# Kernel optimization log

Hardware: AMD Instinct MI355X
Metric: run time of the kernel (lower is better)

The kernel has to match this reference:

```python
import jax, jax.numpy as jnp
import numpy as np


def setup_inputs() -> dict:
    key = jax.random.key(0)
    k1, k2, k3, k4 = jax.random.split(key, 4)
    L, B, D, H = 512, 128, 512, 1024
    x = jax.random.normal(k1, (L, B, D), dtype=jnp.float32)
    Wx = jax.random.normal(k2, (H, D), dtype=jnp.float32) * (1.0 / np.sqrt(D))
    bx = jax.random.normal(k3, (H,), dtype=jnp.float32) * 0.01
    Wh = jax.random.normal(k4, (H, H), dtype=jnp.float32) * (1.0 / np.sqrt(H))
    return {"x": x, "Wx": Wx, "bx": bx, "Wh": Wh}


def reference(x, Wx, bx, Wh):
    # x: [L, B, D]; Wx: [H, D]; bx: [H]; Wh: [H, H]
    # h_t = tanh(x_t @ Wx^T + bx + h_{t-1} @ Wh^T), h_{-1} = 0
    L, B, D = x.shape
    H = Wx.shape[0]
    # Precompute the input projection for all timesteps in one big GEMM.
    xproj = jnp.einsum('lbd,hd->lbh', x, Wx) + bx  # [L, B, H]

    def step(h, xp_t):
        h_new = jnp.tanh(xp_t + h @ Wh.T)  # [B, H]
        return h_new, h_new

    h0 = jnp.zeros((B, H), dtype=x.dtype)
    _, hs = jax.lax.scan(step, h0, xproj)
    return hs  # [L, B, H]
```

## Files before the change

kernel.cpp:

```cpp
#include <hip/hip_runtime.h>
#include <math.h>


#define L_SEQ 512
#define B_SZ  128
#define D_SZ  512
#define H_SZ  1024
#define BH    (B_SZ * H_SZ)

typedef __bf16 bf16x8 __attribute__((ext_vector_type(8)));
typedef float  f32x4  __attribute__((ext_vector_type(4)));
typedef unsigned int uint;

union V8 { bf16x8 b; unsigned short u[8]; uint w[4]; };

__device__ __forceinline__ unsigned short f2bf(float f) {
  unsigned int u = __float_as_uint(f);
  u += 0x7FFFu + ((u >> 16) & 1u);
  return (unsigned short)(u >> 16);
}
__device__ __forceinline__ float bf2f(unsigned short s) {
  return __uint_as_float(((unsigned int)s) << 16);
}

__device__ __forceinline__ float fast_tanh(float x) {
  float e;
  asm("v_exp_f32 %0, %1" : "=v"(e) : "v"(x * 2.885390081777927f));
  float r;
  asm("v_rcp_f32 %0, %1" : "=v"(r) : "v"(e + 1.0f));
  return 1.0f - 2.0f * r;
}

__device__ __forceinline__ void ldg16_sc(bf16x8& d, const unsigned short* p) {
  asm volatile("global_load_dwordx4 %0, %1, off sc0 sc1"
               : "=v"(d) : "v"(p) : "memory");
}
__device__ __forceinline__ void stg2_sc(unsigned short* p, uint v) {
  asm volatile("global_store_short %0, %1, off sc0 sc1"
               :: "v"(p), "v"(v) : "memory");
}
__device__ __forceinline__ void stg4_sc(uint* p, uint v) {
  asm volatile("global_store_dword %0, %1, off sc0 sc1"
               :: "v"(p), "v"(v) : "memory");
}

#define WS_WHH 0
#define WS_WHL 1048576
#define WS_WXH 2097152
#define WS_WXL 2621440
#define WS_HB  3145728
#define WS_CNT 3670016

__global__ void split_kernel(const float* __restrict__ Wh,
                             const float* __restrict__ Wx,
                             unsigned short* __restrict__ ws,
                             unsigned int* __restrict__ flags) {
  if (blockIdx.x == 0) {
    for (int i = threadIdx.x; i < 512; i += 256) flags[i] = 0u;
  }
  const int total = 1048576 + 524288;
  for (int i = blockIdx.x * blockDim.x + threadIdx.x; i < total;
       i += gridDim.x * blockDim.x) {
    const float* src; unsigned short *dh, *dl; int j;
    if (i < 1048576) { src = Wh; dh = ws + WS_WHH; dl = ws + WS_WHL; j = i; }
    else             { src = Wx; dh = ws + WS_WXH; dl = ws + WS_WXL; j = i - 1048576; }
    float v = src[j];
    unsigned short h = f2bf(v);
    dh[j] = h;
    dl[j] = f2bf(v - bf2f(h));
  }
}

__global__ __launch_bounds__(256) void xproj_kernel(
    const float* __restrict__ x,
    const unsigned short* __restrict__ wxh,
    const unsigned short* __restrict__ wxl,
    const float* __restrict__ bx,
    float* __restrict__ out)
{
  const int bid = blockIdx.x;
  const int bn = bid & 15;
  const int bm = bid >> 4;
  const int tid = threadIdx.x;
  const int w = tid >> 6, l = tid & 63;
  const int wm = w & 1, wn = w >> 1;
  const int lr = l & 15, lk = (l >> 4) * 8;
  const int mbase = bm * 128 + wm * 64;
  const int nbase = bn * 64 + wn * 32;

  f32x4 acc[4][2] = {};

  for (int k0 = 0; k0 < 512; k0 += 32) {
    bf16x8 ah[4], al[4], bh[2], bl[2];
#pragma unroll
    for (int i = 0; i < 4; ++i) {
      const float* ap = x + (size_t)(mbase + i * 16 + lr) * 512 + k0 + lk;
      float4 v0 = *reinterpret_cast<const float4*>(ap);
      float4 v1 = *reinterpret_cast<const float4*>(ap + 4);
      float vv[8] = {v0.x, v0.y, v0.z, v0.w, v1.x, v1.y, v1.z, v1.w};
      V8 hh, ll;
#pragma unroll
      for (int e = 0; e < 8; ++e) {
        unsigned short hb = f2bf(vv[e]);
        hh.u[e] = hb;
        ll.u[e] = f2bf(vv[e] - bf2f(hb));
      }
      ah[i] = hh.b; al[i] = ll.b;
    }
#pragma unroll
    for (int j = 0; j < 2; ++j) {
      size_t boff = (size_t)(nbase + j * 16 + lr) * 512 + k0 + lk;
      bh[j] = *reinterpret_cast<const bf16x8*>(wxh + boff);
      bl[j] = *reinterpret_cast<const bf16x8*>(wxl + boff);
    }
#pragma unroll
    for (int i = 0; i < 4; ++i)
#pragma unroll
      for (int j = 0; j < 2; ++j) {
        acc[i][j] = __builtin_amdgcn_mfma_f32_16x16x32_bf16(ah[i], bh[j], acc[i][j], 0, 0, 0);
        acc[i][j] = __builtin_amdgcn_mfma_f32_16x16x32_bf16(ah[i], bl[j], acc[i][j], 0, 0, 0);
        acc[i][j] = __builtin_amdgcn_mfma_f32_16x16x32_bf16(al[i], bh[j], acc[i][j], 0, 0, 0);
      }
  }

#pragma unroll
  for (int j = 0; j < 2; ++j) {
    int n = nbase + j * 16 + lr;
    float bxv = bx[n];
#pragma unroll
    for (int i = 0; i < 4; ++i)
#pragma unroll
      for (int r = 0; r < 4; ++r) {
        int m = mbase + i * 16 + (l >> 4) * 4 + r;
        out[(size_t)m * 1024 + n] = acc[i][j][r] + bxv;
      }
  }
}

__global__ __launch_bounds__(512, 2) void rnn_persistent(
    const unsigned short* __restrict__ whh,
    const unsigned short* __restrict__ whl,
    unsigned short* __restrict__ hb,
    float* __restrict__ out,
    uint* __restrict__ flags)
{
  __shared__ float lds[8 * 32 * 17];
  const int wg = blockIdx.x;
  const int xc = wg & 7, yy = wg >> 3;
  const int mb = xc & 3;
  const int nb = ((xc >> 2) << 5) + yy;
  const int tid = threadIdx.x;
  const int q = tid >> 6;
  const int l = tid & 63;
  const int lr = l & 15, lk = (l >> 4) * 8;
  const int kbase = q * 128 + lk;
  const int row0 = (l >> 4) * 4;

  const unsigned short* bph = whh + (size_t)(nb * 16 + lr) * 1024 + kbase;
  const unsigned short* bpl = whl + (size_t)(nb * 16 + lr) * 1024 + kbase;
  bf16x8 vBh[4], vBl[4];
#pragma unroll
  for (int kb = 0; kb < 4; ++kb) {
    vBh[kb] = *reinterpret_cast<const bf16x8*>(bph + kb * 32);
    vBl[kb] = *reinterpret_cast<const bf16x8*>(bpl + kb * 32);
  }

  const size_t aoff = (size_t)(mb * 32 + lr) * 1024 + kbase;
  const unsigned short* planeA0 = hb + aoff;
  const unsigned short* planeA1 = hb + 2 * BH + aoff;

  const int em = tid >> 4, en = tid & 15;
  const size_t eidx = (size_t)(mb * 32 + em) * 1024 + nb * 16 + en;

  const uint* gate_ptr = flags + (mb << 6) + (q << 3) + (l & 7);
  uint* my_flag = flags + (mb << 6) + nb;

  for (int t = 0; t < L_SEQ; ++t) {
    float* xpt = out + (size_t)t * BH;
    const float xpv = xpt[eidx];
    float hval;

    if (t > 0) {
      const uint tgt = (uint)t;
      for (uint spin = 0; spin < (1u << 22); ++spin) {
        uint f;
        asm volatile("global_load_dword %0, %1, off sc0 sc1\n\t"
                     "s_waitcnt vmcnt(0)"
                     : "=v"(f) : "v"(gate_ptr) : "memory");
        if (__all((int)(f >= tgt))) break;
        __builtin_amdgcn_s_sleep(1);
      }
      __builtin_amdgcn_sched_barrier(0);

      const unsigned short* ah = ((t - 1) & 1) ? planeA1 : planeA0;
      const unsigned short* al = ah + BH;
      bf16x8 vA0h[4], vA0l[4], vA1h[4], vA1l[4];
#pragma unroll
      for (int kb = 0; kb < 4; ++kb) {
        const int ko = kb * 32;
        ldg16_sc(vA0h[kb], ah + ko);
        ldg16_sc(vA0l[kb], al + ko);
        ldg16_sc(vA1h[kb], ah + 16 * 1024 + ko);
        ldg16_sc(vA1l[kb], al + 16 * 1024 + ko);
      }
      asm volatile("s_waitcnt vmcnt(0)" ::: "memory");
      __builtin_amdgcn_sched_barrier(0);

      f32x4 acc0 = {0.f, 0.f, 0.f, 0.f};
      f32x4 acc1 = {0.f, 0.f, 0.f, 0.f};
#pragma unroll
      for (int kb = 0; kb < 4; ++kb) {
        acc0 = __builtin_amdgcn_mfma_f32_16x16x32_bf16(vA0h[kb], vBh[kb], acc0, 0, 0, 0);
        acc1 = __builtin_amdgcn_mfma_f32_16x16x32_bf16(vA1h[kb], vBh[kb], acc1, 0, 0, 0);
        acc0 = __builtin_amdgcn_mfma_f32_16x16x32_bf16(vA0h[kb], vBl[kb], acc0, 0, 0, 0);
        acc1 = __builtin_amdgcn_mfma_f32_16x16x32_bf16(vA1h[kb], vBl[kb], acc1, 0, 0, 0);
        acc0 = __builtin_amdgcn_mfma_f32_16x16x32_bf16(vA0l[kb], vBh[kb], acc0, 0, 0, 0);
        acc1 = __builtin_amdgcn_mfma_f32_16x16x32_bf16(vA1l[kb], vBh[kb], acc1, 0, 0, 0);
      }

#pragma unroll
      for (int r = 0; r < 4; ++r) {
        lds[q * 544 + (row0 + r) * 17 + lr]      = acc0[r];
        lds[q * 544 + (16 + row0 + r) * 17 + lr] = acc1[r];
      }
      __syncthreads();

      float s = 0.f;
#pragma unroll
      for (int qq = 0; qq < 8; ++qq) s += lds[qq * 544 + em * 17 + en];
      hval = fast_tanh(s + xpv);
    } else {
      hval = fast_tanh(xpv);
    }

    unsigned short hhi = f2bf(hval);
    unsigned short hlo = f2bf(hval - bf2f(hhi));
    unsigned short* hcur = hb + (size_t)((t & 1) * 2) * BH;
    stg2_sc(hcur + eidx, (uint)hhi);
    stg2_sc(hcur + BH + eidx, (uint)hlo);
    asm volatile("s_waitcnt vmcnt(0)" ::: "memory");
    __syncthreads();
    if (tid == 0) stg4_sc(my_flag, (uint)(t + 1));

    xpt[eidx] = hval;
  }
}

extern "C" void kernel_launch(void* const* d_in, const int* in_sizes, int n_in,
                              void* d_out, int out_size, void* d_ws, size_t ws_size,
                              hipStream_t stream) {
  const float* x  = (const float*)d_in[0];
  const float* Wx = (const float*)d_in[1];
  const float* bx = (const float*)d_in[2];
  const float* Wh = (const float*)d_in[3];
  float* out = (float*)d_out;
  unsigned short* ws = (unsigned short*)d_ws;

  unsigned short* whh = ws + WS_WHH;
  unsigned short* whl = ws + WS_WHL;
  unsigned short* wxh = ws + WS_WXH;
  unsigned short* wxl = ws + WS_WXL;
  unsigned short* hb  = ws + WS_HB;
  uint* flags         = (uint*)(ws + WS_CNT);

  split_kernel<<<dim3(2048), dim3(256), 0, stream>>>(Wh, Wx, ws, flags);
  xproj_kernel<<<dim3(8192), dim3(256), 0, stream>>>(x, wxh, wxl, bx, out);
  rnn_persistent<<<dim3(256), dim3(512), 0, stream>>>(whh, whl, hb, out, flags);
}
```

Measured before the change: 3.700 ms.

## Interleave two batch chains per workgroup to overlap flag waits with compute

The persistent RNN kernel now launches 128 workgroups instead of 256. Each one owns a column block for two batch slices and alternates between them within each timestep. Gating is split per slice, and flags are published early, so one slice's matmul can proceed while the other slice's dependencies are still arriving. The goal is to hide cross-workgroup synchronization latency, at the cost of halving parallelism, serializing two chains per workgroup, and adding a more delicate flag-ordering protocol. The spin limit is also reduced.

```diff
diff --git a/kernel.cpp b/kernel.cpp
--- a/kernel.cpp
+++ b/kernel.cpp
@@ -4,7 +4,6 @@
 
 #define L_SEQ 512
 #define B_SZ  128
-#define D_SZ  512
 #define H_SZ  1024
 #define BH    (B_SZ * H_SZ)
 
@@ -12,7 +11,7 @@
 typedef float  f32x4  __attribute__((ext_vector_type(4)));
 typedef unsigned int uint;
 
-union V8 { bf16x8 b; unsigned short u[8]; uint w[4]; };
+union V8 { bf16x8 b; unsigned short u[8]; };
 
 __device__ __forceinline__ unsigned short f2bf(float f) {
   unsigned int u = __float_as_uint(f);
@@ -34,6 +33,12 @@
 __device__ __forceinline__ void ldg16_sc(bf16x8& d, const unsigned short* p) {
   asm volatile("global_load_dwordx4 %0, %1, off sc0 sc1"
                : "=v"(d) : "v"(p) : "memory");
+}
+__device__ __forceinline__ uint ld4w_sc(const uint* p) {
+  uint f;
+  asm volatile("global_load_dword %0, %1, off sc0 sc1\n\ts_waitcnt vmcnt(0)"
+               : "=v"(f) : "v"(p) : "memory");
+  return f;
 }
 __device__ __forceinline__ void stg2_sc(unsigned short* p, uint v) {
   asm volatile("global_store_short %0, %1, off sc0 sc1"
@@ -146,9 +151,9 @@
 {
   __shared__ float lds[8 * 32 * 17];
   const int wg = blockIdx.x;
-  const int xc = wg & 7, yy = wg >> 3;
-  const int mb = xc & 3;
-  const int nb = ((xc >> 2) << 5) + yy;
+  const int p  = wg & 1;
+  const int nb = wg >> 1;
+  const int mbA = 2 * p, mbB = 2 * p + 1;
   const int tid = threadIdx.x;
   const int q = tid >> 6;
   const int l = tid & 63;
@@ -165,84 +170,102 @@
     vBl[kb] = *reinterpret_cast<const bf16x8*>(bpl + kb * 32);
   }
 
-  const size_t aoff = (size_t)(mb * 32 + lr) * 1024 + kbase;
-  const unsigned short* planeA0 = hb + aoff;
-  const unsigned short* planeA1 = hb + 2 * BH + aoff;
-
+  const size_t aoffA = (size_t)(mbA * 32 + lr) * 1024 + kbase;
+  const size_t aoffB = (size_t)(mbB * 32 + lr) * 1024 + kbase;
   const int em = tid >> 4, en = tid & 15;
-  const size_t eidx = (size_t)(mb * 32 + em) * 1024 + nb * 16 + en;
-
-  const uint* gate_ptr = flags + (mb << 6) + (q << 3) + (l & 7);
-  uint* my_flag = flags + (mb << 6) + nb;
-
-  for (int t = 0; t < L_SEQ; ++t) {
-    float* xpt = out + (size_t)t * BH;
-    const float xpv = xpt[eidx];
-    float hval;
-
-    if (t > 0) {
-      const uint tgt = (uint)t;
-      for (uint spin = 0; spin < (1u << 22); ++spin) {
-        uint f;
-        asm volatile("global_load_dword %0, %1, off sc0 sc1\n\t"
-                     "s_waitcnt vmcnt(0)"
-                     : "=v"(f) : "v"(gate_ptr) : "memory");
-        if (__all((int)(f >= tgt))) break;
-        __builtin_amdgcn_s_sleep(1);
-      }
-      __builtin_amdgcn_sched_barrier(0);
-
-      const unsigned short* ah = ((t - 1) & 1) ? planeA1 : planeA0;
-      const unsigned short* al = ah + BH;
-      bf16x8 vA0h[4], vA0l[4], vA1h[4], vA1l[4];
-#pragma unroll
-      for (int kb = 0; kb < 4; ++kb) {
-        const int ko = kb * 32;
-        ldg16_sc(vA0h[kb], ah + ko);
-        ldg16_sc(vA0l[kb], al + ko);
-        ldg16_sc(vA1h[kb], ah + 16 * 1024 + ko);
-        ldg16_sc(vA1l[kb], al + 16 * 1024 + ko);
-      }
-      asm volatile("s_waitcnt vmcnt(0)" ::: "memory");
-      __builtin_amdgcn_sched_barrier(0);
-
-      f32x4 acc0 = {0.f, 0.f, 0.f, 0.f};
-      f32x4 acc1 = {0.f, 0.f, 0.f, 0.f};
-#pragma unroll
-      for (int kb = 0; kb < 4; ++kb) {
-        acc0 = __builtin_amdgcn_mfma_f32_16x16x32_bf16(vA0h[kb], vBh[kb], acc0, 0, 0, 0);
-        acc1 = __builtin_amdgcn_mfma_f32_16x16x32_bf16(vA1h[kb], vBh[kb], acc1, 0, 0, 0);
-        acc0 = __builtin_amdgcn_mfma_f32_16x16x32_bf16(vA0h[kb], vBl[kb], acc0, 0, 0, 0);
-        acc1 = __builtin_amdgcn_mfma_f32_16x16x32_bf16(vA1h[kb], vBl[kb], acc1, 0, 0, 0);
-        acc0 = __builtin_amdgcn_mfma_f32_16x16x32_bf16(vA0l[kb], vBh[kb], acc0, 0, 0, 0);
-        acc1 = __builtin_amdgcn_mfma_f32_16x16x32_bf16(vA1l[kb], vBh[kb], acc1, 0, 0, 0);
-      }
-
-#pragma unroll
-      for (int r = 0; r < 4; ++r) {
-        lds[q * 544 + (row0 + r) * 17 + lr]      = acc0[r];
-        lds[q * 544 + (16 + row0 + r) * 17 + lr] = acc1[r];
-      }
-      __syncthreads();
-
-      float s = 0.f;
-#pragma unroll
-      for (int qq = 0; qq < 8; ++qq) s += lds[qq * 544 + em * 17 + en];
-      hval = fast_tanh(s + xpv);
-    } else {
-      hval = fast_tanh(xpv);
-    }
-
-    unsigned short hhi = f2bf(hval);
-    unsigned short hlo = f2bf(hval - bf2f(hhi));
+  const size_t eidxA = (size_t)(mbA * 32 + em) * 1024 + nb * 16 + en;
+  const size_t eidxB = (size_t)(mbB * 32 + em) * 1024 + nb * 16 + en;
+  const uint* gateA = flags + (mbA << 6) + (q << 3) + (l & 7);
+  const uint* gateB = flags + (mbB << 6) + (q << 3) + (l & 7);
+  uint* myA = flags + (mbA << 6) + nb;
+  uint* myB = flags + (mbB << 6) + nb;
+
+  auto chain_mm = [&](const size_t aoff, int t, float xpv) -> float {
+    const unsigned short* ah = hb + (size_t)(((t - 1) & 1) * 2) * BH + aoff;
+    const unsigned short* al = ah + BH;
+    bf16x8 vA0h[4], vA0l[4], vA1h[4], vA1l[4];
+#pragma unroll
+    for (int kb = 0; kb < 4; ++kb) {
+      const int ko = kb * 32;
+      ldg16_sc(vA0h[kb], ah + ko);
+      ldg16_sc(vA0l[kb], al + ko);
+      ldg16_sc(vA1h[kb], ah + 16 * 1024 + ko);
+      ldg16_sc(vA1l[kb], al + 16 * 1024 + ko);
+    }
+    asm volatile("s_waitcnt vmcnt(0)" ::: "memory");
+    __builtin_amdgcn_sched_barrier(0);
+
+    f32x4 a0 = {0.f, 0.f, 0.f, 0.f};
+    f32x4 a1 = {0.f, 0.f, 0.f, 0.f};
+#pragma unroll
+    for (int kb = 0; kb < 4; ++kb) {
+      a0 = __builtin_amdgcn_mfma_f32_16x16x32_bf16(vA0h[kb], vBh[kb], a0, 0, 0, 0);
+      a1 = __builtin_amdgcn_mfma_f32_16x16x32_bf16(vA1h[kb], vBh[kb], a1, 0, 0, 0);
+      a0 = __builtin_amdgcn_mfma_f32_16x16x32_bf16(vA0h[kb], vBl[kb], a0, 0, 0, 0);
+      a1 = __builtin_amdgcn_mfma_f32_16x16x32_bf16(vA1h[kb], vBl[kb], a1, 0, 0, 0);
+      a0 = __builtin_amdgcn_mfma_f32_16x16x32_bf16(vA0l[kb], vBh[kb], a0, 0, 0, 0);
+      a1 = __builtin_amdgcn_mfma_f32_16x16x32_bf16(vA1l[kb], vBh[kb], a1, 0, 0, 0);
+    }
+#pragma unroll
+    for (int r = 0; r < 4; ++r) {
+      lds[q * 544 + (row0 + r) * 17 + lr]      = a0[r];
+      lds[q * 544 + (16 + row0 + r) * 17 + lr] = a1[r];
+    }
+    __syncthreads();
+    float s = 0.f;
+#pragma unroll
+    for (int qq = 0; qq < 8; ++qq) s += lds[qq * 544 + em * 17 + en];
+    return fast_tanh(s + xpv);
+  };
+
+  auto store_h = [&](int t, size_t eidx, float h) {
+    unsigned short hhi = f2bf(h);
+    unsigned short hlo = f2bf(h - bf2f(hhi));
     unsigned short* hcur = hb + (size_t)((t & 1) * 2) * BH;
     stg2_sc(hcur + eidx, (uint)hhi);
     stg2_sc(hcur + BH + eidx, (uint)hlo);
+  };
+
+  auto gate = [&](const uint* gp, uint tgt) {
+    for (uint spin = 0; spin < (1u << 20); ++spin) {
+      uint f = ld4w_sc(gp);
+      if (__all((int)(f >= tgt))) break;
+      __builtin_amdgcn_s_sleep(1);
+    }
+    __builtin_amdgcn_sched_barrier(0);
+  };
+
+  {
+    float hA = fast_tanh(out[eidxA]);
+    float hB = fast_tanh(out[eidxB]);
+    store_h(0, eidxA, hA);
+    store_h(0, eidxB, hB);
+    out[eidxA] = hA;
+    out[eidxB] = hB;
     asm volatile("s_waitcnt vmcnt(0)" ::: "memory");
     __syncthreads();
-    if (tid == 0) stg4_sc(my_flag, (uint)(t + 1));
-
-    xpt[eidx] = hval;
+    if (tid == 0) { stg4_sc(myA, 1u); stg4_sc(myB, 1u); }
+  }
+
+  for (int t = 1; t < L_SEQ; ++t) {
+    float* xpt = out + (size_t)t * BH;
+    const float xpvA = xpt[eidxA];
+    const float xpvB = xpt[eidxB];
+
+    gate(gateA, (uint)t);
+    __syncthreads();
+    if (tid == 0) stg4_sc(myB, (uint)t);
+    float hA = chain_mm(aoffA, t, xpvA);
+    store_h(t, eidxA, hA);
+
+    gate(gateB, (uint)t);
+    __syncthreads();
+    if (tid == 0) stg4_sc(myA, (uint)(t + 1));
+    float hB = chain_mm(aoffB, t, xpvB);
+    store_h(t, eidxB, hB);
+
+    xpt[eidxA] = hA;
+    xpt[eidxB] = hB;
   }
 }
 
@@ -265,5 +288,5 @@
 
   split_kernel<<<dim3(2048), dim3(256), 0, stream>>>(Wh, Wx, ws, flags);
   xproj_kernel<<<dim3(8192), dim3(256), 0, stream>>>(x, wxh, wxl, bx, out);
-  rnn_persistent<<<dim3(256), dim3(512), 0, stream>>>(whh, whl, hb, out, flags);
-}
+  rnn_persistent<<<dim3(128), dim3(512), 0, stream>>>(whh, whl, hb, out, flags);
+}
```

New measurement: 5.773 ms. 56.0% more time.

## Replace flag barriers with timestep-tagged hidden-state words polled directly

Applied to the files above, without the earlier changes.

Each hidden-state element is now stored as an 8-byte word: the packed bf16 hi/lo pair plus the timestep tag. Consumers poll the data itself until every tag matches, which removes the separate flag store and flag poll round trip from each step. Work is redistributed across 128 workgroups, each owning 16 batch rows by 64 hidden columns over the full K. Fetched rows are transposed into LDS, MFMAs run per wave, and partial sums are reduced through LDS. The tag buffer reuses the Wx split region. This adds per-step polling traffic, and correctness depends on stale tags never matching the current timestep.

```diff
diff --git a/kernel.cpp b/kernel.cpp
--- a/kernel.cpp
+++ b/kernel.cpp
@@ -4,23 +4,25 @@
 
 #define L_SEQ 512
 #define B_SZ  128
-#define D_SZ  512
 #define H_SZ  1024
 #define BH    (B_SZ * H_SZ)
 
 typedef __bf16 bf16x8 __attribute__((ext_vector_type(8)));
 typedef float  f32x4  __attribute__((ext_vector_type(4)));
 typedef unsigned int uint;
-
-union V8 { bf16x8 b; unsigned short u[8]; uint w[4]; };
-
-__device__ __forceinline__ unsigned short f2bf(float f) {
-  unsigned int u = __float_as_uint(f);
+typedef uint u32x4 __attribute__((ext_vector_type(4)));
+typedef uint u32x2 __attribute__((ext_vector_type(2)));
+typedef unsigned short ushort;
+
+union V8 { bf16x8 b; ushort u[8]; };
+
+__device__ __forceinline__ ushort f2bf(float f) {
+  uint u = __float_as_uint(f);
   u += 0x7FFFu + ((u >> 16) & 1u);
-  return (unsigned short)(u >> 16);
-}
-__device__ __forceinline__ float bf2f(unsigned short s) {
-  return __uint_as_float(((unsigned int)s) << 16);
+  return (ushort)(u >> 16);
+}
+__device__ __forceinline__ float bf2f(ushort s) {
+  return __uint_as_float(((uint)s) << 16);
 }
 
 __device__ __forceinline__ float fast_tanh(float x) {
@@ -31,16 +33,12 @@
   return 1.0f - 2.0f * r;
 }
 
-__device__ __forceinline__ void ldg16_sc(bf16x8& d, const unsigned short* p) {
+__device__ __forceinline__ void ldg16_sc(u32x4& d, const uint* p) {
   asm volatile("global_load_dwordx4 %0, %1, off sc0 sc1"
                : "=v"(d) : "v"(p) : "memory");
 }
-__device__ __forceinline__ void stg2_sc(unsigned short* p, uint v) {
-  asm volatile("global_store_short %0, %1, off sc0 sc1"
-               :: "v"(p), "v"(v) : "memory");
-}
-__device__ __forceinline__ void stg4_sc(uint* p, uint v) {
-  asm volatile("global_store_dword %0, %1, off sc0 sc1"
+__device__ __forceinline__ void stg8_sc(uint* p, u32x2 v) {
+  asm volatile("global_store_dwordx2 %0, %1, off sc0 sc1"
                :: "v"(p), "v"(v) : "memory");
 }
 
@@ -48,24 +46,18 @@
 #define WS_WHL 1048576
 #define WS_WXH 2097152
 #define WS_WXL 2621440
-#define WS_HB  3145728
-#define WS_CNT 3670016
 
 __global__ void split_kernel(const float* __restrict__ Wh,
                              const float* __restrict__ Wx,
-                             unsigned short* __restrict__ ws,
-                             unsigned int* __restrict__ flags) {
-  if (blockIdx.x == 0) {
-    for (int i = threadIdx.x; i < 512; i += 256) flags[i] = 0u;
-  }
+                             ushort* __restrict__ ws) {
   const int total = 1048576 + 524288;
   for (int i = blockIdx.x * blockDim.x + threadIdx.x; i < total;
        i += gridDim.x * blockDim.x) {
-    const float* src; unsigned short *dh, *dl; int j;
+    const float* src; ushort *dh, *dl; int j;
     if (i < 1048576) { src = Wh; dh = ws + WS_WHH; dl = ws + WS_WHL; j = i; }
     else             { src = Wx; dh = ws + WS_WXH; dl = ws + WS_WXL; j = i - 1048576; }
     float v = src[j];
-    unsigned short h = f2bf(v);
+    ushort h = f2bf(v);
     dh[j] = h;
     dl[j] = f2bf(v - bf2f(h));
   }
@@ -73,8 +65,8 @@
 
 __global__ __launch_bounds__(256) void xproj_kernel(
     const float* __restrict__ x,
-    const unsigned short* __restrict__ wxh,
-    const unsigned short* __restrict__ wxl,
+    const ushort* __restrict__ wxh,
+    const ushort* __restrict__ wxl,
     const float* __restrict__ bx,
     float* __restrict__ out)
 {
@@ -101,7 +93,7 @@
       V8 hh, ll;
 #pragma unroll
       for (int e = 0; e < 8; ++e) {
-        unsigned short hb = f2bf(vv[e]);
+        ushort hb = f2bf(vv[e]);
         hh.u[e] = hb;
         ll.u[e] = f2bf(vv[e] - bf2f(hb));
       }
@@ -138,111 +130,133 @@
 }
 
 __global__ __launch_bounds__(512, 2) void rnn_persistent(
-    const unsigned short* __restrict__ whh,
-    const unsigned short* __restrict__ whl,
-    unsigned short* __restrict__ hb,
-    float* __restrict__ out,
-    uint* __restrict__ flags)
+    const ushort* __restrict__ whh,
+    const ushort* __restrict__ whl,
+    uint* __restrict__ hbt,
+    float* __restrict__ out)
 {
-  __shared__ float lds[8 * 32 * 17];
+  __shared__ uint smraw[16384];
+  ushort* lds_hi = (ushort*)smraw;
+  ushort* lds_lo = lds_hi + 16384;
+  float*  part   = (float*)smraw;
+
   const int wg = blockIdx.x;
-  const int xc = wg & 7, yy = wg >> 3;
-  const int mb = xc & 3;
-  const int nb = ((xc >> 2) << 5) + yy;
+  const int g  = wg & 7;
+  const int c  = wg >> 3;
   const int tid = threadIdx.x;
-  const int q = tid >> 6;
-  const int l = tid & 63;
-  const int lr = l & 15, lk = (l >> 4) * 8;
-  const int kbase = q * 128 + lk;
-  const int row0 = (l >> 4) * 4;
-
-  const unsigned short* bph = whh + (size_t)(nb * 16 + lr) * 1024 + kbase;
-  const unsigned short* bpl = whl + (size_t)(nb * 16 + lr) * 1024 + kbase;
-  bf16x8 vBh[4], vBl[4];
-#pragma unroll
-  for (int kb = 0; kb < 4; ++kb) {
-    vBh[kb] = *reinterpret_cast<const bf16x8*>(bph + kb * 32);
-    vBl[kb] = *reinterpret_cast<const bf16x8*>(bpl + kb * 32);
-  }
-
-  const size_t aoff = (size_t)(mb * 32 + lr) * 1024 + kbase;
-  const unsigned short* planeA0 = hb + aoff;
-  const unsigned short* planeA1 = hb + 2 * BH + aoff;
-
-  const int em = tid >> 4, en = tid & 15;
-  const size_t eidx = (size_t)(mb * 32 + em) * 1024 + nb * 16 + en;
-
-  const uint* gate_ptr = flags + (mb << 6) + (q << 3) + (l & 7);
-  uint* my_flag = flags + (mb << 6) + nb;
-
-  for (int t = 0; t < L_SEQ; ++t) {
+  const int w = tid >> 6, l = tid & 63;
+  const int lr = l & 15, lq = l >> 4;
+
+  bf16x8 vBh[4][4], vBl[4][4];
+#pragma unroll
+  for (int ct = 0; ct < 4; ++ct)
+#pragma unroll
+    for (int ck = 0; ck < 4; ++ck) {
+      size_t a = (size_t)(c * 64 + ct * 16 + lr) * 1024 + w * 128 + ck * 32 + lq * 8;
+      vBh[ct][ck] = *reinterpret_cast<const bf16x8*>(whh + a);
+      vBl[ct][ck] = *reinterpret_cast<const bf16x8*>(whl + a);
+    }
+
+  const int e0 = tid * 2;
+  const int row0 = e0 >> 6, cw0 = e0 & 63;
+  const int row1 = (e0 + 1) >> 6, cw1 = (e0 + 1) & 63;
+  const size_t oidx0 = (size_t)(g * 16 + row0) * 1024 + c * 64 + cw0;
+  const size_t oidx1 = (size_t)(g * 16 + row1) * 1024 + c * 64 + cw1;
+
+  const uint* pollbase[2];
+  pollbase[0] = hbt + (((size_t)g * 16384 + w * 2048 + l * 2) << 1);
+  pollbase[1] = hbt + (((size_t)BH + g * 16384 + w * 2048 + l * 2) << 1);
+
+  {
+    float h0 = fast_tanh(out[oidx0]);
+    float h1 = fast_tanh(out[oidx1]);
+    out[oidx0] = h0;
+    out[oidx1] = h1;
+    ushort hh0 = f2bf(h0), hh1 = f2bf(h1);
+    u32x2 v0, v1;
+    v0[0] = ((uint)hh0 << 16) | (uint)f2bf(h0 - bf2f(hh0)); v0[1] = 1u;
+    v1[0] = ((uint)hh1 << 16) | (uint)f2bf(h1 - bf2f(hh1)); v1[1] = 1u;
+    stg8_sc(hbt + (oidx0 << 1), v0);
+    stg8_sc(hbt + (oidx1 << 1), v1);
+  }
+
+  for (int t = 1; t < L_SEQ; ++t) {
     float* xpt = out + (size_t)t * BH;
-    const float xpv = xpt[eidx];
-    float hval;
-
-    if (t > 0) {
-      const uint tgt = (uint)t;
-      for (uint spin = 0; spin < (1u << 22); ++spin) {
-        uint f;
-        asm volatile("global_load_dword %0, %1, off sc0 sc1\n\t"
-                     "s_waitcnt vmcnt(0)"
-                     : "=v"(f) : "v"(gate_ptr) : "memory");
-        if (__all((int)(f >= tgt))) break;
-        __builtin_amdgcn_s_sleep(1);
-      }
-      __builtin_amdgcn_sched_barrier(0);
-
-      const unsigned short* ah = ((t - 1) & 1) ? planeA1 : planeA0;
-      const unsigned short* al = ah + BH;
-      bf16x8 vA0h[4], vA0l[4], vA1h[4], vA1l[4];
-#pragma unroll
-      for (int kb = 0; kb < 4; ++kb) {
-        const int ko = kb * 32;
-        ldg16_sc(vA0h[kb], ah + ko);
-        ldg16_sc(vA0l[kb], al + ko);
-        ldg16_sc(vA1h[kb], ah + 16 * 1024 + ko);
-        ldg16_sc(vA1l[kb], al + 16 * 1024 + ko);
-      }
+    const float xpv0 = xpt[oidx0];
+    const float xpv1 = xpt[oidx1];
+
+    const uint* pb = pollbase[(t - 1) & 1];
+    const uint tg = (uint)t;
+    u32x4 d[16];
+    for (uint spin = 0; spin < (1u << 20); ++spin) {
+      #pragma unroll
+      for (int i = 0; i < 16; ++i) ldg16_sc(d[i], pb + (i << 8));
       asm volatile("s_waitcnt vmcnt(0)" ::: "memory");
       __builtin_amdgcn_sched_barrier(0);
-
-      f32x4 acc0 = {0.f, 0.f, 0.f, 0.f};
-      f32x4 acc1 = {0.f, 0.f, 0.f, 0.f};
-#pragma unroll
-      for (int kb = 0; kb < 4; ++kb) {
-        acc0 = __builtin_amdgcn_mfma_f32_16x16x32_bf16(vA0h[kb], vBh[kb], acc0, 0, 0, 0);
-        acc1 = __builtin_amdgcn_mfma_f32_16x16x32_bf16(vA1h[kb], vBh[kb], acc1, 0, 0, 0);
-        acc0 = __builtin_amdgcn_mfma_f32_16x16x32_bf16(vA0h[kb], vBl[kb], acc0, 0, 0, 0);
-        acc1 = __builtin_amdgcn_mfma_f32_16x16x32_bf16(vA1h[kb], vBl[kb], acc1, 0, 0, 0);
-        acc0 = __builtin_amdgcn_mfma_f32_16x16x32_bf16(vA0l[kb], vBh[kb], acc0, 0, 0, 0);
-        acc1 = __builtin_amdgcn_mfma_f32_16x16x32_bf16(vA1l[kb], vBh[kb], acc1, 0, 0, 0);
-      }
-
-#pragma unroll
-      for (int r = 0; r < 4; ++r) {
-        lds[q * 544 + (row0 + r) * 17 + lr]      = acc0[r];
-        lds[q * 544 + (16 + row0 + r) * 17 + lr] = acc1[r];
-      }
-      __syncthreads();
-
-      float s = 0.f;
-#pragma unroll
-      for (int qq = 0; qq < 8; ++qq) s += lds[qq * 544 + em * 17 + en];
-      hval = fast_tanh(s + xpv);
-    } else {
-      hval = fast_tanh(xpv);
-    }
-
-    unsigned short hhi = f2bf(hval);
-    unsigned short hlo = f2bf(hval - bf2f(hhi));
-    unsigned short* hcur = hb + (size_t)((t & 1) * 2) * BH;
-    stg2_sc(hcur + eidx, (uint)hhi);
-    stg2_sc(hcur + BH + eidx, (uint)hlo);
-    asm volatile("s_waitcnt vmcnt(0)" ::: "memory");
+      bool ok = true;
+      #pragma unroll
+      for (int i = 0; i < 16; ++i) ok = ok && (d[i][1] == tg) && (d[i][3] == tg);
+      if (__all((int)ok)) break;
+      __builtin_amdgcn_s_sleep(1);
+    }
+    __builtin_amdgcn_sched_barrier(0);
+
+    #pragma unroll
+    for (int i = 0; i < 16; ++i) {
+      const int e = w * 2048 + i * 128 + l * 2;
+      const int row = e >> 10, k = e & 1023;
+      const int u = ((k >> 3) << 4) + row;
+      const int pos = k & 7;
+      uint hip = (d[i][0] >> 16) | (d[i][2] & 0xFFFF0000u);
+      uint lop = (d[i][0] & 0xFFFFu) | (d[i][2] << 16);
+      *reinterpret_cast<uint*>(lds_hi + u * 8 + pos) = hip;
+      *reinterpret_cast<uint*>(lds_lo + u * 8 + pos) = lop;
+    }
     __syncthreads();
-    if (tid == 0) stg4_sc(my_flag, (uint)(t + 1));
-
-    xpt[eidx] = hval;
+
+    bf16x8 vAh[4], vAl[4];
+    #pragma unroll
+    for (int ck = 0; ck < 4; ++ck) {
+      const int u = ((w * 16 + ck * 4 + lq) << 4) + lr;
+      vAh[ck] = *reinterpret_cast<const bf16x8*>(lds_hi + u * 8);
+      vAl[ck] = *reinterpret_cast<const bf16x8*>(lds_lo + u * 8);
+    }
+    __syncthreads();
+
+    f32x4 acc[4] = {};
+    #pragma unroll
+    for (int ct = 0; ct < 4; ++ct)
+      #pragma unroll
+      for (int ck = 0; ck < 4; ++ck) {
+        acc[ct] = __builtin_amdgcn_mfma_f32_16x16x32_bf16(vAh[ck], vBh[ct][ck], acc[ct], 0, 0, 0);
+        acc[ct] = __builtin_amdgcn_mfma_f32_16x16x32_bf16(vAh[ck], vBl[ct][ck], acc[ct], 0, 0, 0);
+        acc[ct] = __builtin_amdgcn_mfma_f32_16x16x32_bf16(vAl[ck], vBh[ct][ck], acc[ct], 0, 0, 0);
+      }
+
+    #pragma unroll
+    for (int ct = 0; ct < 4; ++ct)
+      #pragma unroll
+      for (int r = 0; r < 4; ++r)
+        part[w * 1088 + (ct * 16 + lr) * 17 + lq * 4 + r] = acc[ct][r];
+    __syncthreads();
+
+    float s0 = 0.f, s1 = 0.f;
+    #pragma unroll
+    for (int q = 0; q < 8; ++q) {
+      s0 += part[q * 1088 + cw0 * 17 + row0];
+      s1 += part[q * 1088 + cw1 * 17 + row1];
+    }
+    float h0 = fast_tanh(s0 + xpv0);
+    float h1 = fast_tanh(s1 + xpv1);
+    ushort hh0 = f2bf(h0), hh1 = f2bf(h1);
+    u32x2 v0, v1;
+    v0[0] = ((uint)hh0 << 16) | (uint)f2bf(h0 - bf2f(hh0)); v0[1] = tg + 1u;
+    v1[0] = ((uint)hh1 << 16) | (uint)f2bf(h1 - bf2f(hh1)); v1[1] = tg + 1u;
+    uint* planew = hbt + ((size_t)(t & 1) * BH << 1);
+    stg8_sc(planew + (oidx0 << 1), v0);
+    stg8_sc(planew + (oidx1 << 1), v1);
+    xpt[oidx0] = h0;
+    xpt[oidx1] = h1;
   }
 }
 
@@ -254,16 +268,15 @@
   const float* bx = (const float*)d_in[2];
   const float* Wh = (const float*)d_in[3];
   float* out = (float*)d_out;
-  unsigned short* ws = (unsigned short*)d_ws;
-
-  unsigned short* whh = ws + WS_WHH;
-  unsigned short* whl = ws + WS_WHL;
-  unsigned short* wxh = ws + WS_WXH;
-  unsigned short* wxl = ws + WS_WXL;
-  unsigned short* hb  = ws + WS_HB;
-  uint* flags         = (uint*)(ws + WS_CNT);
-
-  split_kernel<<<dim3(2048), dim3(256), 0, stream>>>(Wh, Wx, ws, flags);
+  ushort* ws = (ushort*)d_ws;
+
+  ushort* whh = ws + WS_WHH;
+  ushort* whl = ws + WS_WHL;
+  ushort* wxh = ws + WS_WXH;
+  ushort* wxl = ws + WS_WXL;
+  uint*   hbt = (uint*)(ws + WS_WXH);
+
+  split_kernel<<<dim3(2048), dim3(256), 0, stream>>>(Wh, Wx, ws);
   xproj_kernel<<<dim3(8192), dim3(256), 0, stream>>>(x, wxh, wxl, bx, out);
-  rnn_persistent<<<dim3(256), dim3(512), 0, stream>>>(whh, whl, hb, out, flags);
-}
+  rnn_persistent<<<dim3(128), dim3(512), 0, stream>>>(whh, whl, hbt, out);
+}
```

Result: slower. 4.150 ms (+12.2%).

## Fuse input projection GEMM into persistent RNN kernel with per-timestep readiness flags

Applied to the files above, without the earlier changes.

Merges the input-projection GEMM and the persistent recurrence into one launch. The first 256 blocks run the recurrence; the remaining blocks compute projection tiles in timestep order and publish a flag per tile. Recurrence blocks spin on both the neighbour step flags and the matching projection flag before reading that step's projection. The aim is to overlap the projection with the early timesteps and drop a kernel boundary. The projection blocks share CUs with the latency-bound recurrence and may slow its steps, and the design relies on the persistent blocks all being resident while the producer blocks still make progress.

```diff
diff --git a/kernel.cpp b/kernel.cpp
--- a/kernel.cpp
+++ b/kernel.cpp
@@ -4,23 +4,23 @@
 
 #define L_SEQ 512
 #define B_SZ  128
-#define D_SZ  512
 #define H_SZ  1024
 #define BH    (B_SZ * H_SZ)
 
 typedef __bf16 bf16x8 __attribute__((ext_vector_type(8)));
 typedef float  f32x4  __attribute__((ext_vector_type(4)));
 typedef unsigned int uint;
-
-union V8 { bf16x8 b; unsigned short u[8]; uint w[4]; };
-
-__device__ __forceinline__ unsigned short f2bf(float f) {
-  unsigned int u = __float_as_uint(f);
+typedef unsigned short ushort;
+
+union V8 { bf16x8 b; ushort u[8]; uint w[4]; };
+
+__device__ __forceinline__ ushort f2bf(float f) {
+  uint u = __float_as_uint(f);
   u += 0x7FFFu + ((u >> 16) & 1u);
-  return (unsigned short)(u >> 16);
-}
-__device__ __forceinline__ float bf2f(unsigned short s) {
-  return __uint_as_float(((unsigned int)s) << 16);
+  return (ushort)(u >> 16);
+}
+__device__ __forceinline__ float bf2f(ushort s) {
+  return __uint_as_float(((uint)s) << 16);
 }
 
 __device__ __forceinline__ float fast_tanh(float x) {
@@ -31,11 +31,11 @@
   return 1.0f - 2.0f * r;
 }
 
-__device__ __forceinline__ void ldg16_sc(bf16x8& d, const unsigned short* p) {
+__device__ __forceinline__ void ldg16_sc(bf16x8& d, const ushort* p) {
   asm volatile("global_load_dwordx4 %0, %1, off sc0 sc1"
                : "=v"(d) : "v"(p) : "memory");
 }
-__device__ __forceinline__ void stg2_sc(unsigned short* p, uint v) {
+__device__ __forceinline__ void stg2_sc(ushort* p, uint v) {
   asm volatile("global_store_short %0, %1, off sc0 sc1"
                :: "v"(p), "v"(v) : "memory");
 }
@@ -49,115 +49,108 @@
 #define WS_WXH 2097152
 #define WS_WXL 2621440
 #define WS_HB  3145728
-#define WS_CNT 3670016
+#define WS_FLG 3670016
 
 __global__ void split_kernel(const float* __restrict__ Wh,
                              const float* __restrict__ Wx,
-                             unsigned short* __restrict__ ws,
-                             unsigned int* __restrict__ flags) {
-  if (blockIdx.x == 0) {
-    for (int i = threadIdx.x; i < 512; i += 256) flags[i] = 0u;
-  }
+                             ushort* __restrict__ ws,
+                             uint* __restrict__ flg) {
+  const int gid = blockIdx.x * blockDim.x + threadIdx.x;
+  if (gid < 256 + 8192) flg[gid] = 0u;
   const int total = 1048576 + 524288;
-  for (int i = blockIdx.x * blockDim.x + threadIdx.x; i < total;
-       i += gridDim.x * blockDim.x) {
-    const float* src; unsigned short *dh, *dl; int j;
+  for (int i = gid; i < total; i += gridDim.x * blockDim.x) {
+    const float* src; ushort *dh, *dl; int j;
     if (i < 1048576) { src = Wh; dh = ws + WS_WHH; dl = ws + WS_WHL; j = i; }
     else             { src = Wx; dh = ws + WS_WXH; dl = ws + WS_WXL; j = i - 1048576; }
     float v = src[j];
-    unsigned short h = f2bf(v);
+    ushort h = f2bf(v);
     dh[j] = h;
     dl[j] = f2bf(v - bf2f(h));
   }
 }
 
-__global__ __launch_bounds__(256) void xproj_kernel(
+__global__ __launch_bounds__(512, 4) void fused_kernel(
     const float* __restrict__ x,
-    const unsigned short* __restrict__ wxh,
-    const unsigned short* __restrict__ wxl,
+    const ushort* __restrict__ wxh,
+    const ushort* __restrict__ wxl,
     const float* __restrict__ bx,
-    float* __restrict__ out)
+    const ushort* __restrict__ whh,
+    const ushort* __restrict__ whl,
+    ushort* __restrict__ hb,
+    float* __restrict__ out,
+    uint* __restrict__ flags,
+    uint* __restrict__ xpflags)
 {
+  __shared__ float lds[8 * 32 * 17];
   const int bid = blockIdx.x;
-  const int bn = bid & 15;
-  const int bm = bid >> 4;
   const int tid = threadIdx.x;
-  const int w = tid >> 6, l = tid & 63;
-  const int wm = w & 1, wn = w >> 1;
-  const int lr = l & 15, lk = (l >> 4) * 8;
-  const int mbase = bm * 128 + wm * 64;
-  const int nbase = bn * 64 + wn * 32;
-
-  f32x4 acc[4][2] = {};
-
-  for (int k0 = 0; k0 < 512; k0 += 32) {
-    bf16x8 ah[4], al[4], bh[2], bl[2];
-#pragma unroll
-    for (int i = 0; i < 4; ++i) {
-      const float* ap = x + (size_t)(mbase + i * 16 + lr) * 512 + k0 + lk;
-      float4 v0 = *reinterpret_cast<const float4*>(ap);
-      float4 v1 = *reinterpret_cast<const float4*>(ap + 4);
-      float vv[8] = {v0.x, v0.y, v0.z, v0.w, v1.x, v1.y, v1.z, v1.w};
-      V8 hh, ll;
-#pragma unroll
-      for (int e = 0; e < 8; ++e) {
-        unsigned short hb = f2bf(vv[e]);
-        hh.u[e] = hb;
-        ll.u[e] = f2bf(vv[e] - bf2f(hb));
-      }
-      ah[i] = hh.b; al[i] = ll.b;
+
+  if (bid >= 256) {
+    const int xb = bid - 256;
+    const int bn = xb & 15;
+    const int bm = xb >> 4;
+    const int w = tid >> 6, l = tid & 63;
+    const int wm = w & 1, wn = w >> 1;
+    const int lr = l & 15, lk = (l >> 4) * 8;
+    const int mbase = bm * 128 + wm * 64;
+    const int nbase = bn * 64 + wn * 16;
+
+    f32x4 acc[4] = {};
+    for (int k0 = 0; k0 < 512; k0 += 32) {
+      bf16x8 ah[4], al[4], bh, bl;
+#pragma unroll
+      for (int i = 0; i < 4; ++i) {
+        const float* ap = x + (size_t)(mbase + i * 16 + lr) * 512 + k0 + lk;
+        float4 v0 = *reinterpret_cast<const float4*>(ap);
+        float4 v1 = *reinterpret_cast<const float4*>(ap + 4);
+        float vv[8] = {v0.x, v0.y, v0.z, v0.w, v1.x, v1.y, v1.z, v1.w};
+        V8 hh, ll;
+#pragma unroll
+        for (int e = 0; e < 8; ++e) {
+          ushort hbv = f2bf(vv[e]);
+          hh.u[e] = hbv;
+          ll.u[e] = f2bf(vv[e] - bf2f(hbv));
+        }
+        ah[i] = hh.b; al[i] = ll.b;
+      }
+      size_t boff = (size_t)(nbase + lr) * 512 + k0 + lk;
+      bh = *reinterpret_cast<const bf16x8*>(wxh + boff);
+      bl = *reinterpret_cast<const bf16x8*>(wxl + boff);
+#pragma unroll
+      for (int i = 0; i < 4; ++i) {
+        acc[i] = __builtin_amdgcn_mfma_f32_16x16x32_bf16(ah[i], bh, acc[i], 0, 0, 0);
+        acc[i] = __builtin_amdgcn_mfma_f32_16x16x32_bf16(ah[i], bl, acc[i], 0, 0, 0);
+        acc[i] = __builtin_amdgcn_mfma_f32_16x16x32_bf16(al[i], bh, acc[i], 0, 0, 0);
+      }
     }
-#pragma unroll
-    for (int j = 0; j < 2; ++j) {
-      size_t boff = (size_t)(nbase + j * 16 + lr) * 512 + k0 + lk;
-      bh[j] = *reinterpret_cast<const bf16x8*>(wxh + boff);
-      bl[j] = *reinterpret_cast<const bf16x8*>(wxl + boff);
-    }
-#pragma unroll
-    for (int i = 0; i < 4; ++i)
-#pragma unroll
-      for (int j = 0; j < 2; ++j) {
-        acc[i][j] = __builtin_amdgcn_mfma_f32_16x16x32_bf16(ah[i], bh[j], acc[i][j], 0, 0, 0);
-        acc[i][j] = __builtin_amdgcn_mfma_f32_16x16x32_bf16(ah[i], bl[j], acc[i][j], 0, 0, 0);
-        acc[i][j] = __builtin_amdgcn_mfma_f32_16x16x32_bf16(al[i], bh[j], acc[i][j], 0, 0, 0);
-      }
-  }
-
-#pragma unroll
-  for (int j = 0; j < 2; ++j) {
-    int n = nbase + j * 16 + lr;
-    float bxv = bx[n];
+    const int n = nbase + lr;
+    const float bxv = bx[n];
 #pragma unroll
     for (int i = 0; i < 4; ++i)
 #pragma unroll
       for (int r = 0; r < 4; ++r) {
         int m = mbase + i * 16 + (l >> 4) * 4 + r;
-        out[(size_t)m * 1024 + n] = acc[i][j][r] + bxv;
-      }
-  }
-}
-
-__global__ __launch_bounds__(512, 2) void rnn_persistent(
-    const unsigned short* __restrict__ whh,
-    const unsigned short* __restrict__ whl,
-    unsigned short* __restrict__ hb,
-    float* __restrict__ out,
-    uint* __restrict__ flags)
-{
-  __shared__ float lds[8 * 32 * 17];
-  const int wg = blockIdx.x;
+        stg4_sc((uint*)(out + (size_t)m * 1024 + n),
+                __float_as_uint(acc[i][r] + bxv));
+      }
+    asm volatile("s_waitcnt vmcnt(0)" ::: "memory");
+    __syncthreads();
+    if (tid == 0) stg4_sc(xpflags + bm * 16 + bn, 1u);
+    return;
+  }
+
+  const int wg = bid;
   const int xc = wg & 7, yy = wg >> 3;
   const int mb = xc & 3;
   const int nb = ((xc >> 2) << 5) + yy;
-  const int tid = threadIdx.x;
   const int q = tid >> 6;
   const int l = tid & 63;
   const int lr = l & 15, lk = (l >> 4) * 8;
   const int kbase = q * 128 + lk;
   const int row0 = (l >> 4) * 4;
 
-  const unsigned short* bph = whh + (size_t)(nb * 16 + lr) * 1024 + kbase;
-  const unsigned short* bpl = whl + (size_t)(nb * 16 + lr) * 1024 + kbase;
+  const ushort* bph = whh + (size_t)(nb * 16 + lr) * 1024 + kbase;
+  const ushort* bpl = whl + (size_t)(nb * 16 + lr) * 1024 + kbase;
   bf16x8 vBh[4], vBl[4];
 #pragma unroll
   for (int kb = 0; kb < 4; ++kb) {
@@ -166,8 +159,8 @@
   }
 
   const size_t aoff = (size_t)(mb * 32 + lr) * 1024 + kbase;
-  const unsigned short* planeA0 = hb + aoff;
-  const unsigned short* planeA1 = hb + 2 * BH + aoff;
+  const ushort* planeA0 = hb + aoff;
+  const ushort* planeA1 = hb + 2 * BH + aoff;
 
   const int em = tid >> 4, en = tid & 15;
   const size_t eidx = (size_t)(mb * 32 + em) * 1024 + nb * 16 + en;
@@ -176,24 +169,44 @@
   uint* my_flag = flags + (mb << 6) + nb;
 
   for (int t = 0; t < L_SEQ; ++t) {
-    float* xpt = out + (size_t)t * BH;
-    const float xpv = xpt[eidx];
+    const uint* xpf_ptr = xpflags + t * 16 + (nb >> 2);
     float hval;
 
-    if (t > 0) {
-      const uint tgt = (uint)t;
-      for (uint spin = 0; spin < (1u << 22); ++spin) {
-        uint f;
+    if (t == 0) {
+      for (uint spin = 0; spin < (1u << 20); ++spin) {
+        uint xf;
         asm volatile("global_load_dword %0, %1, off sc0 sc1\n\t"
                      "s_waitcnt vmcnt(0)"
-                     : "=v"(f) : "v"(gate_ptr) : "memory");
-        if (__all((int)(f >= tgt))) break;
+                     : "=v"(xf) : "v"(xpf_ptr) : "memory");
+        if (__all((int)(xf != 0u))) break;
         __builtin_amdgcn_s_sleep(1);
       }
       __builtin_amdgcn_sched_barrier(0);
-
-      const unsigned short* ah = ((t - 1) & 1) ? planeA1 : planeA0;
-      const unsigned short* al = ah + BH;
+      uint xu;
+      asm volatile("global_load_dword %0, %1, off sc0 sc1\n\t"
+                   "s_waitcnt vmcnt(0)"
+                   : "=v"(xu) : "v"((const uint*)(out + eidx)) : "memory");
+      hval = fast_tanh(__uint_as_float(xu));
+    } else {
+      const uint tgt = (uint)t;
+      for (uint spin = 0; spin < (1u << 20); ++spin) {
+        uint f, xf;
+        asm volatile("global_load_dword %0, %2, off sc0 sc1\n\t"
+                     "global_load_dword %1, %3, off sc0 sc1\n\t"
+                     "s_waitcnt vmcnt(0)"
+                     : "=&v"(f), "=&v"(xf)
+                     : "v"(gate_ptr), "v"(xpf_ptr) : "memory");
+        if (__all((int)((f >= tgt) & (xf != 0u)))) break;
+        __builtin_amdgcn_s_sleep(1);
+      }
+      __builtin_amdgcn_sched_barrier(0);
+
+      uint xu;
+      asm volatile("global_load_dword %0, %1, off sc0 sc1"
+                   : "=v"(xu)
+                   : "v"((const uint*)(out + (size_t)t * BH + eidx)) : "memory");
+      const ushort* ah = ((t - 1) & 1) ? planeA1 : planeA0;
+      const ushort* al = ah + BH;
       bf16x8 vA0h[4], vA0l[4], vA1h[4], vA1l[4];
 #pragma unroll
       for (int kb = 0; kb < 4; ++kb) {
@@ -228,21 +241,19 @@
       float s = 0.f;
 #pragma unroll
       for (int qq = 0; qq < 8; ++qq) s += lds[qq * 544 + em * 17 + en];
-      hval = fast_tanh(s + xpv);
-    } else {
-      hval = fast_tanh(xpv);
+      hval = fast_tanh(s + __uint_as_float(xu));
     }
 
-    unsigned short hhi = f2bf(hval);
-    unsigned short hlo = f2bf(hval - bf2f(hhi));
-    unsigned short* hcur = hb + (size_t)((t & 1) * 2) * BH;
+    ushort hhi = f2bf(hval);
+    ushort hlo = f2bf(hval - bf2f(hhi));
+    ushort* hcur = hb + (size_t)((t & 1) * 2) * BH;
     stg2_sc(hcur + eidx, (uint)hhi);
     stg2_sc(hcur + BH + eidx, (uint)hlo);
     asm volatile("s_waitcnt vmcnt(0)" ::: "memory");
     __syncthreads();
     if (tid == 0) stg4_sc(my_flag, (uint)(t + 1));
 
-    xpt[eidx] = hval;
+    out[(size_t)t * BH + eidx] = hval;
   }
 }
 
@@ -254,16 +265,17 @@
   const float* bx = (const float*)d_in[2];
   const float* Wh = (const float*)d_in[3];
   float* out = (float*)d_out;
-  unsigned short* ws = (unsigned short*)d_ws;
-
-  unsigned short* whh = ws + WS_WHH;
-  unsigned short* whl = ws + WS_WHL;
-  unsigned short* wxh = ws + WS_WXH;
-  unsigned short* wxl = ws + WS_WXL;
-  unsigned short* hb  = ws + WS_HB;
-  uint* flags         = (uint*)(ws + WS_CNT);
+  ushort* ws = (ushort*)d_ws;
+
+  ushort* whh = ws + WS_WHH;
+  ushort* whl = ws + WS_WHL;
+  ushort* wxh = ws + WS_WXH;
+  ushort* wxl = ws + WS_WXL;
+  ushort* hb  = ws + WS_HB;
+  uint* flags   = (uint*)(ws + WS_FLG);
+  uint* xpflags = flags + 256;
 
   split_kernel<<<dim3(2048), dim3(256), 0, stream>>>(Wh, Wx, ws, flags);
-  xproj_kernel<<<dim3(8192), dim3(256), 0, stream>>>(x, wxh, wxl, bx, out);
-  rnn_persistent<<<dim3(256), dim3(512), 0, stream>>>(whh, whl, hb, out, flags);
-}
+  fused_kernel<<<dim3(256 + 8192), dim3(512), 0, stream>>>(
+      x, wxh, wxl, bx, whh, whl, hb, out, flags, xpflags);
+}
```

Result: slower. 5.005 ms (+35.3%).
